# Optimization experiments

Measured on AMD Instinct MI355X. Metric: run time of the kernel, lower is better.

The kernel has to match this reference:

```python
import jax, jax.numpy as jnp
import numpy as np

B, N, C = 16, 577, 768
H, D = 12, 64
HID = 3072
EPS = 1e-5


def setup_inputs() -> dict:
    key = jax.random.key(0)
    ks = jax.random.split(key, 5)
    s = 0.02
    return {
        "x": jax.random.normal(ks[0], (B, N, C), jnp.float32),
        "w_qkv": jax.random.normal(ks[1], (C, 3 * C), jnp.float32) * s,
        "b_qkv": jnp.zeros((3 * C,), jnp.float32),
        "w_proj": jax.random.normal(ks[2], (C, C), jnp.float32) * s,
        "b_proj": jnp.zeros((C,), jnp.float32),
        "g1": jnp.ones((C,), jnp.float32),
        "be1": jnp.zeros((C,), jnp.float32),
        "g2": jnp.ones((C,), jnp.float32),
        "be2": jnp.zeros((C,), jnp.float32),
        "w1": jax.random.normal(ks[3], (C, HID), jnp.float32) * s,
        "b1": jnp.zeros((HID,), jnp.float32),
        "w2": jax.random.normal(ks[4], (HID, C), jnp.float32) * s,
        "b2": jnp.zeros((C,), jnp.float32),
    }


def _layernorm(x, g, b):
    mu = jnp.mean(x, axis=-1, keepdims=True)
    var = jnp.mean(jnp.square(x - mu), axis=-1, keepdims=True)
    return (x - mu) * jax.lax.rsqrt(var + EPS) * g + b


def reference(x, w_qkv, b_qkv, w_proj, b_proj, g1, be1, g2, be2, w1, b1, w2, b2):
    # --- pre-norm MHA ---
    xn = _layernorm(x, g1, be1)
    qkv = xn @ w_qkv + b_qkv                      # [B,N,3C]
    qkv = qkv.reshape(B, N, 3, H, D).transpose(2, 0, 3, 1, 4)  # [3,B,H,N,D]
    q, k, v = qkv[0], qkv[1], qkv[2]
    scale = 1.0 / jnp.sqrt(jnp.float32(D))
    scores = jnp.einsum("bhnd,bhmd->bhnm", q, k) * scale
    attn_weights = jax.nn.softmax(scores, axis=-1)  # [B,H,N,N]
    ctx = jnp.einsum("bhnm,bhmd->bhnd", attn_weights, v)
    ctx = ctx.transpose(0, 2, 1, 3).reshape(B, N, C)
    attn_out = ctx @ w_proj + b_proj
    x = x + attn_out
    # --- MLP (exact GELU, matching nn.GELU default) ---
    h = _layernorm(x, g2, be2) @ w1 + b1
    h = jax.nn.gelu(h, approximate=False)
    x = x + (h @ w2 + b2)
    return x, attn_weights
```

## Files before the change

### kernel.cpp

```cpp
#include <hip/hip_runtime.h>
#include <hip/hip_bf16.h>
#include <cmath>

constexpr int B_ = 16, N_ = 577, C_ = 768, H_ = 12, D_ = 64, HID_ = 3072;
constexpr int ROWS_ = B_ * N_;
constexpr int BH_ = B_ * H_;
constexpr int KVT_ = 10;
constexpr int QBLK_ = 10;

typedef __attribute__((ext_vector_type(8))) __bf16 bf16x8;
typedef __attribute__((ext_vector_type(4))) float f32x4;
typedef __attribute__((ext_vector_type(4), aligned(4))) float f32x4u;

#define DEVI __device__ __forceinline__

DEVI unsigned short f2bf(float f) {
  unsigned u = __float_as_uint(f);
  return (unsigned short)((u + 0x7fffu + ((u >> 16) & 1u)) >> 16);
}
DEVI float bf2f(unsigned short u) { return __uint_as_float(((unsigned)u) << 16); }

DEVI void gload16(const void* src, void* dst) {
  __builtin_amdgcn_global_load_lds(
      (const __attribute__((address_space(1))) char*)src,
      (__attribute__((address_space(3))) char*)dst, 16, 0, 0);
}
#define VMCNT0 asm volatile("s_waitcnt vmcnt(0)" ::: "memory")
#define FENCE asm volatile("" ::: "memory")
#define RAWBAR do { FENCE; __builtin_amdgcn_s_barrier(); FENCE; } while (0)

__global__ __launch_bounds__(256) void cvtT_kernel(const float* __restrict__ in,
                                                   unsigned short* __restrict__ out,
                                                   int K, int N) {
  __shared__ float t[64][65];
  int n0 = blockIdx.x * 64, k0 = blockIdx.y * 64;
  int tx = threadIdx.x & 63, ty = threadIdx.x >> 6;
#pragma unroll
  for (int r = 0; r < 16; r++) {
    int kr = ty * 16 + r;
    t[kr][tx] = in[(long)(k0 + kr) * N + n0 + tx];
  }
  __syncthreads();
#pragma unroll
  for (int r = 0; r < 16; r++) {
    int nr = ty * 16 + r;
    out[(long)(n0 + nr) * K + k0 + tx] = f2bf(t[tx][nr]);
  }
}

__global__ __launch_bounds__(256) void ln_kernel(const float* __restrict__ x,
                                                 const float* __restrict__ g,
                                                 const float* __restrict__ be,
                                                 unsigned short* __restrict__ out) {
  int row = blockIdx.x;
  const float* xr = x + (long)row * C_;
  float v[3];
  float s = 0.f, s2 = 0.f;
#pragma unroll
  for (int j = 0; j < 3; j++) {
    int i = threadIdx.x + j * 256;
    v[j] = xr[i];
    s += v[j];
    s2 += v[j] * v[j];
  }
#pragma unroll
  for (int o = 32; o > 0; o >>= 1) {
    s += __shfl_down(s, o);
    s2 += __shfl_down(s2, o);
  }
  __shared__ float sh[8];
  int w = threadIdx.x >> 6;
  if ((threadIdx.x & 63) == 0) { sh[w] = s; sh[4 + w] = s2; }
  __syncthreads();
  s = sh[0] + sh[1] + sh[2] + sh[3];
  s2 = sh[4] + sh[5] + sh[6] + sh[7];
  float mu = s * (1.f / C_);
  float var = s2 * (1.f / C_) - mu * mu;
  float rs = rsqrtf(var + 1e-5f);
#pragma unroll
  for (int j = 0; j < 3; j++) {
    int i = threadIdx.x + j * 256;
    out[(long)row * C_ + i] = f2bf((v[j] - mu) * rs * g[i] + be[i]);
  }
}

__global__ __launch_bounds__(256) void attn_kernel(
    const unsigned short* __restrict__ qg,
    const unsigned short* __restrict__ kg,
    const unsigned short* __restrict__ vt,
    float* __restrict__ attn,
    unsigned short* __restrict__ ctx) {
  __shared__ unsigned short KVs[2][2][64][64];
  __shared__ unsigned short Ps[4][16][72];
  const int wgid = (blockIdx.x & 7) * (BH_ * QBLK_ / 8) + (blockIdx.x >> 3);
  const int bh = wgid / QBLK_, qb = wgid % QBLK_;
  const int b = bh / H_, h = bh % H_;
  const int tid = threadIdx.x, wave = tid >> 6, lane = tid & 63;
  const int l15 = lane & 15, l4 = lane >> 4;
  const int q0w = qb * 64 + wave * 16;

  const unsigned short* Qh = qg + (long)bh * N_ * D_;
  const char* Kb = (const char*)(kg + (long)bh * N_ * D_);
  const char* Vb = (const char*)(vt + (long)bh * D_ * N_);

  int qrc = q0w + l15; if (qrc >= N_) qrc = N_ - 1;
  bf16x8 qa0 = *(const bf16x8*)(Qh + (long)qrc * D_ + l4 * 8);
  bf16x8 qa1 = *(const bf16x8*)(Qh + (long)qrc * D_ + 32 + l4 * 8);

  auto stage = [&](int buf, int which, const char* g0, int rstride) {
#pragma unroll
    for (int i = 0; i < 2; i++) {
      int off = i * 4096 + tid * 16;
      int row = off >> 7, colD = off & 127;
      const char* src = g0 + (long)row * rstride + (colD ^ ((row & 7) << 4));
      char* dst = ((char*)KVs) + buf * 16384 + which * 8192 + i * 4096 + wave * 1024;
      gload16(src, dst);
    }
  };
  auto rdKV = [&](int buf, int which, int row, int colb) -> bf16x8 {
    const char* p = ((const char*)KVs) + buf * 16384 + which * 8192 + row * 128 +
                    (colb ^ ((row & 7) << 4));
    return *(const bf16x8*)p;
  };
  auto computeS = [&](int buf, int kv0, f32x4 (&s)[4]) {
#pragma unroll
    for (int nf = 0; nf < 4; nf++) {
      int row = nf * 16 + l15;
      bf16x8 k0v = rdKV(buf, 0, row, l4 * 16);
      bf16x8 k1v = rdKV(buf, 0, row, 64 + l4 * 16);
      f32x4 z = {0.f, 0.f, 0.f, 0.f};
      z = __builtin_amdgcn_mfma_f32_16x16x32_bf16(qa0, k0v, z, 0, 0, 0);
      z = __builtin_amdgcn_mfma_f32_16x16x32_bf16(qa1, k1v, z, 0, 0, 0);
      if (kv0 + row >= N_) z = f32x4{-1e30f, -1e30f, -1e30f, -1e30f};
      s[nf] = z;
    }
  };

  float m_ln[4], l_ln[4];
#pragma unroll
  for (int r = 0; r < 4; r++) { m_ln[r] = -1e30f; l_ln[r] = 0.f; }

  stage(0, 0, Kb, 128);
  VMCNT0; __syncthreads();
  int buf = 0;
  for (int kt = 0; kt < KVT_; kt++) {
    if (kt + 1 < KVT_) stage(buf ^ 1, 0, Kb + (long)(kt + 1) * 8192, 128);
    f32x4 s[4];
    computeS(buf, kt * 64, s);
#pragma unroll
    for (int r = 0; r < 4; r++) {
      float t0 = fmaxf(fmaxf(s[0][r], s[1][r]), fmaxf(s[2][r], s[3][r]));
      float mn = fmaxf(m_ln[r], t0);
      float sc = __expf(m_ln[r] - mn);
      l_ln[r] = l_ln[r] * sc + __expf(s[0][r] - mn) + __expf(s[1][r] - mn) +
                __expf(s[2][r] - mn) + __expf(s[3][r] - mn);
      m_ln[r] = mn;
    }
    VMCNT0; __syncthreads();
    buf ^= 1;
  }

  float m_run[4], inv_l[4];
#pragma unroll
  for (int r = 0; r < 4; r++) {
    float m = m_ln[r];
#pragma unroll
    for (int o = 1; o < 16; o <<= 1) m = fmaxf(m, __shfl_xor(m, o));
    float li = l_ln[r] * __expf(m_ln[r] - m);
#pragma unroll
    for (int o = 1; o < 16; o <<= 1) li += __shfl_xor(li, o);
    m_run[r] = m;
    inv_l[r] = 1.f / li;
  }

  f32x4 cacc[4];
#pragma unroll
  for (int nf = 0; nf < 4; nf++) cacc[nf] = f32x4{0.f, 0.f, 0.f, 0.f};

  stage(0, 0, Kb, 128);
  stage(0, 1, Vb, N_ * 2);
  VMCNT0; __syncthreads();
  buf = 0;
  for (int kt = 0; kt < KVT_; kt++) {
    const int kv0 = kt * 64;
    if (kt + 1 < KVT_) {
      stage(buf ^ 1, 0, Kb + (long)(kt + 1) * 8192, 128);
      stage(buf ^ 1, 1, Vb + (long)(kt + 1) * 128, N_ * 2);
    }
    f32x4 s[4];
    computeS(buf, kv0, s);
#pragma unroll
    for (int nf = 0; nf < 4; nf++)
#pragma unroll
      for (int r = 0; r < 4; r++) {
        float p = __expf(s[nf][r] - m_run[r]) * inv_l[r];
        Ps[wave][l4 * 4 + r][nf * 16 + l15] = f2bf(p);
      }
    if (kt < KVT_ - 1) {
      int prow = lane >> 4;
      int c0 = (lane & 15) * 4;
#pragma unroll
      for (int rg = 0; rg < 4; rg++) {
        int row = rg * 4 + prow;
        int qv = q0w + row;
        if (qv < N_) {
          ushort4 pb = *(const ushort4*)&Ps[wave][row][c0];
          f32x4u f;
          f[0] = bf2f(pb.x); f[1] = bf2f(pb.y); f[2] = bf2f(pb.z); f[3] = bf2f(pb.w);
          __builtin_nontemporal_store(
              f, (f32x4u*)(attn + ((long)bh * N_ + qv) * N_ + kv0 + c0));
        }
      }
    } else {
      if ((lane & 15) == 0) {
        int prow = lane >> 4;
#pragma unroll
        for (int rg = 0; rg < 4; rg++) {
          int row = rg * 4 + prow;
          int qv = q0w + row;
          if (qv < N_)
            __builtin_nontemporal_store(bf2f(Ps[wave][row][0]),
                                        attn + ((long)bh * N_ + qv) * N_ + 576);
        }
      }
    }
#pragma unroll
    for (int ks = 0; ks < 2; ks++) {
      bf16x8 pa = *(const bf16x8*)&Ps[wave][l15][ks * 32 + l4 * 8];
#pragma unroll
      for (int nf = 0; nf < 4; nf++) {
        bf16x8 vb = rdKV(buf, 1, nf * 16 + l15, ks * 64 + l4 * 16);
        cacc[nf] = __builtin_amdgcn_mfma_f32_16x16x32_bf16(pa, vb, cacc[nf], 0, 0, 0);
      }
    }
    VMCNT0; __syncthreads();
    buf ^= 1;
  }

#pragma unroll
  for (int nf = 0; nf < 4; nf++)
#pragma unroll
    for (int r = 0; r < 4; r++) {
      int qv = q0w + l4 * 4 + r;
      if (qv >= N_) continue;
      int d = nf * 16 + l15;
      ctx[((long)b * N_ + qv) * C_ + h * D_ + d] = f2bf(cacc[nf][r]);
    }
}

template <int EPI>
__global__ __launch_bounds__(256) void gemm128(
    const unsigned short* __restrict__ A,
    const unsigned short* __restrict__ BT,
    int M, int K, int Nc,
    void* __restrict__ outp, const float* __restrict__ bias,
    const float* __restrict__ resid) {
  __shared__ unsigned short As[2][128][64];
  __shared__ unsigned short Bs[2][128][64];
  const int tid = threadIdx.x, wave = tid >> 6, lane = tid & 63;
  const int l15 = lane & 15, l4 = lane >> 4;
  const long m0 = (long)blockIdx.y * 128, n0 = (long)blockIdx.x * 128;
  const int wr = (wave >> 1) * 64, wc = (wave & 1) * 64;

  f32x4 acc[4][4];
#pragma unroll
  for (int i = 0; i < 4; i++)
#pragma unroll
    for (int j = 0; j < 4; j++) acc[i][j] = f32x4{0.f, 0.f, 0.f, 0.f};

  auto stageA = [&](int buf, int t) {
#pragma unroll
    for (int i = 0; i < 4; i++) {
      int off = i * 4096 + tid * 16;
      int row = off >> 7, colD = off & 127;
      long gr = m0 + row; if (gr >= M) gr = M - 1;
      const char* src = (const char*)A + (gr * (long)K + (long)t * 64) * 2 +
                        (colD ^ ((row & 7) << 4));
      char* dst = ((char*)As) + buf * 16384 + i * 4096 + wave * 1024;
      gload16(src, dst);
    }
  };
  auto stageB = [&](int buf, int t) {
#pragma unroll
    for (int i = 0; i < 4; i++) {
      int off = i * 4096 + tid * 16;
      int row = off >> 7, colD = off & 127;
      const char* src = (const char*)BT + ((n0 + row) * (long)K + (long)t * 64) * 2 +
                        (colD ^ ((row & 7) << 4));
      char* dst = ((char*)Bs) + buf * 16384 + i * 4096 + wave * 1024;
      gload16(src, dst);
    }
  };

  const int nt = K / 64;
  stageA(0, 0); stageB(0, 0);
  VMCNT0; __syncthreads();
  int buf = 0;
  for (int t = 0; t < nt; t++) {
    if (t + 1 < nt) { stageA(buf ^ 1, t + 1); stageB(buf ^ 1, t + 1); }
    bf16x8 af[4][2], bfr[4][2];
#pragma unroll
    for (int mf = 0; mf < 4; mf++)
#pragma unroll
      for (int kk = 0; kk < 2; kk++) {
        int row = wr + mf * 16 + l15, colb = kk * 64 + l4 * 16;
        af[mf][kk] = *(const bf16x8*)(((const char*)As) + buf * 16384 + row * 128 +
                                      (colb ^ ((row & 7) << 4)));
      }
#pragma unroll
    for (int nf = 0; nf < 4; nf++)
#pragma unroll
      for (int kk = 0; kk < 2; kk++) {
        int row = wc + nf * 16 + l15, colb = kk * 64 + l4 * 16;
        bfr[nf][kk] = *(const bf16x8*)(((const char*)Bs) + buf * 16384 + row * 128 +
                                       (colb ^ ((row & 7) << 4)));
      }
#pragma unroll
    for (int kk = 0; kk < 2; kk++)
#pragma unroll
      for (int mf = 0; mf < 4; mf++)
#pragma unroll
        for (int nf = 0; nf < 4; nf++)
          acc[mf][nf] =
              __builtin_amdgcn_mfma_f32_16x16x32_bf16(af[mf][kk], bfr[nf][kk], acc[mf][nf], 0, 0, 0);
    VMCNT0; __syncthreads();
    buf ^= 1;
  }

#pragma unroll
  for (int mf = 0; mf < 4; mf++)
#pragma unroll
    for (int nf = 0; nf < 4; nf++)
#pragma unroll
      for (int r = 0; r < 4; r++) {
        long row = m0 + wr + mf * 16 + l4 * 4 + r;
        long col = n0 + wc + nf * 16 + l15;
        if (row >= M) continue;
        float v = acc[mf][nf][r];
        if constexpr (EPI == 3 || EPI == 5) {
          float* o = (float*)outp;
          long idx = row * (long)Nc + col;
          o[idx] = v + bias[col] + resid[idx];
        } else if constexpr (EPI == 4) {
          v += bias[col];
          float ge = 0.5f * v * (1.f + erff(v * 0.70710678118654752f));
          ((unsigned short*)outp)[row * (long)Nc + col] = f2bf(ge);
        }
      }
}

template <int EPI>
__global__ __launch_bounds__(512, 2) void gemm256(
    const unsigned short* __restrict__ A,
    const unsigned short* __restrict__ BT,
    int M, int K, int Nc,
    void* __restrict__ outp, const float* __restrict__ bias,
    const float* __restrict__ resid) {
  __shared__ unsigned short smem[2][2][2][128][64];
  const int tid = threadIdx.x, wave = tid >> 6, lane = tid & 63;
  const int l15 = lane & 15, l4 = lane >> 4;
  const int wm = wave >> 2, wn = wave & 3;

  const int nbx = gridDim.x;
  const int nwg = nbx * gridDim.y;
  int orig = blockIdx.y * nbx + blockIdx.x;
  int qq = nwg >> 3, r8 = nwg & 7;
  int xcd = orig & 7, idx = orig >> 3;
  int wg = (xcd < r8 ? xcd * (qq + 1) : r8 * (qq + 1) + (xcd - r8) * qq) + idx;
  const long m0 = (long)(wg / nbx) * 256;
  const long n0 = (long)(wg % nbx) * 256;

  f32x4 acc[2][2][4][2];
#pragma unroll
  for (int a = 0; a < 2; a++)
#pragma unroll
    for (int b = 0; b < 2; b++)
#pragma unroll
      for (int m = 0; m < 4; m++)
#pragma unroll
        for (int n = 0; n < 2; n++) acc[a][b][m][n] = f32x4{0.f, 0.f, 0.f, 0.f};

  auto stage = [&](int d, int op, int half, int t) {
#pragma unroll
    for (int it = 0; it < 2; it++) {
      int off = it * 8192 + tid * 16;
      int lrow = off >> 7, colb = off & 127;
      long grow;
      if (op == 0) {
        grow = m0 + half * 128 + lrow;
        if (grow >= M) grow = M - 1;
      } else {
        grow = n0 + half * 128 + lrow;
      }
      const unsigned short* gp = (op == 0) ? A : BT;
      const char* src = (const char*)(gp + grow * (long)K + (long)t * 64) +
                        (colb ^ ((lrow & 7) << 4));
      char* dst = ((char*)smem) + (((d * 2 + op) * 2 + half) * 16384) + off;
      gload16(src, dst);
    }
  };
  auto rdfrag = [&](int d, int op, int half, int lr, int kk) -> bf16x8 {
    const char* p = ((const char*)smem) + (((d * 2 + op) * 2 + half) * 16384) + lr * 128 +
                    ((kk * 64 + l4 * 16) ^ ((lr & 7) << 4));
    return *(const bf16x8*)p;
  };

  bf16x8 av[4][2];

#define PHASE(d, qm, qn, STAGECODE, VMCODE)                                              \
  {                                                                                      \
    if constexpr (qn == 0) {                                                             \
      _Pragma("unroll") for (int m = 0; m < 4; m++)                                      \
          _Pragma("unroll") for (int kk = 0; kk < 2; kk++)                               \
              av[m][kk] = rdfrag(d, 0, qm, wm * 64 + m * 16 + l15, kk);                  \
    }                                                                                    \
    bf16x8 bv[2][2];                                                                     \
    _Pragma("unroll") for (int n = 0; n < 2; n++)                                        \
        _Pragma("unroll") for (int kk = 0; kk < 2; kk++)                                 \
            bv[n][kk] = rdfrag(d, 1, qn, wn * 32 + n * 16 + l15, kk);                    \
    STAGECODE;                                                                           \
    VMCODE;                                                                              \
    RAWBAR;                                                                              \
    __builtin_amdgcn_s_setprio(1);                                                       \
    _Pragma("unroll") for (int kk = 0; kk < 2; kk++)                                     \
        _Pragma("unroll") for (int m = 0; m < 4; m++)                                    \
            _Pragma("unroll") for (int n = 0; n < 2; n++)                                \
                acc[qm][qn][m][n] = __builtin_amdgcn_mfma_f32_16x16x32_bf16(             \
                    av[m][kk], bv[n][kk], acc[qm][qn][m][n], 0, 0, 0);                   \
    __builtin_amdgcn_s_setprio(0);                                                       \
    RAWBAR;                                                                              \
  }

  const int nt = K / 64, ni = nt / 2;
  stage(0, 0, 0, 0); stage(0, 0, 1, 0); stage(0, 1, 0, 0); stage(0, 1, 1, 0);
  stage(1, 0, 0, 1); stage(1, 0, 1, 1); stage(1, 1, 0, 1); stage(1, 1, 1, 1);
  asm volatile("s_waitcnt vmcnt(8)" ::: "memory");
  RAWBAR;

  for (int i = 0; i < ni; i++) {
    const int t1 = 2 * i + 1, t2 = 2 * i + 2, t3 = 2 * i + 3;
    PHASE(0, 0, 0, { if (i > 0) stage(1, 0, 1, t1); }, {});
    PHASE(0, 0, 1, { if (i > 0) stage(1, 1, 1, t1); }, {});
    PHASE(0, 1, 0, { if (t2 < nt) stage(0, 0, 0, t2); }, {});
    PHASE(0, 1, 1, { if (t2 < nt) stage(0, 1, 0, t2); },
          { if (t2 < nt) { asm volatile("s_waitcnt vmcnt(4)" ::: "memory"); }
            else { asm volatile("s_waitcnt vmcnt(0)" ::: "memory"); } });
    PHASE(1, 0, 0, { if (t2 < nt) stage(0, 0, 1, t2); }, {});
    PHASE(1, 0, 1, { if (t2 < nt) stage(0, 1, 1, t2); }, {});
    PHASE(1, 1, 0, { if (t3 < nt) stage(1, 0, 0, t3); }, {});
    PHASE(1, 1, 1, { if (t3 < nt) stage(1, 1, 0, t3); },
          { if (t3 < nt) { asm volatile("s_waitcnt vmcnt(4)" ::: "memory"); }
            else { asm volatile("s_waitcnt vmcnt(0)" ::: "memory"); } });
  }
#undef PHASE

#pragma unroll
  for (int qm = 0; qm < 2; qm++)
#pragma unroll
    for (int qn = 0; qn < 2; qn++)
#pragma unroll
      for (int m = 0; m < 4; m++)
#pragma unroll
        for (int n = 0; n < 2; n++)
#pragma unroll
          for (int r = 0; r < 4; r++) {
            long row = m0 + qm * 128 + wm * 64 + m * 16 + l4 * 4 + r;
            long col = n0 + qn * 128 + wn * 32 + n * 16 + l15;
            if (row >= M) continue;
            float v = acc[qm][qn][m][n][r];
            if constexpr (EPI == 0) {
              v += bias[col];
              int which = (int)col / C_;
              int rem = (int)col % C_;
              int hh = rem >> 6, d = rem & 63;
              int bb = (int)row / N_, nn = (int)row % N_;
              if (which == 0) v *= 0.125f;
              unsigned short* o = (unsigned short*)outp;
              long base = (long)which * ((long)BH_ * N_ * D_);
              long oidx;
              if (which < 2)
                oidx = base + (((long)(bb * H_ + hh)) * N_ + nn) * D_ + d;
              else
                oidx = base + (((long)(bb * H_ + hh)) * D_ + d) * N_ + nn;
              o[oidx] = f2bf(v);
            } else if constexpr (EPI == 4) {
              v += bias[col];
              float ge = 0.5f * v * (1.f + erff(v * 0.70710678118654752f));
              ((unsigned short*)outp)[row * (long)Nc + col] = f2bf(ge);
            } else {
              float* o = (float*)outp;
              long oidx = row * (long)Nc + col;
              o[oidx] = v + bias[col] + resid[oidx];
            }
          }
}

extern "C" void kernel_launch(void* const* d_in, const int* in_sizes, int n_in,
                              void* d_out, int out_size, void* d_ws, size_t ws_size,
                              hipStream_t stream) {
  const float* x = (const float*)d_in[0];
  const float* w_qkv = (const float*)d_in[1];
  const float* b_qkv = (const float*)d_in[2];
  const float* w_proj = (const float*)d_in[3];
  const float* b_proj = (const float*)d_in[4];
  const float* g1 = (const float*)d_in[5];
  const float* be1 = (const float*)d_in[6];
  const float* g2 = (const float*)d_in[7];
  const float* be2 = (const float*)d_in[8];
  const float* w1 = (const float*)d_in[9];
  const float* b1 = (const float*)d_in[10];
  const float* w2 = (const float*)d_in[11];
  const float* b2 = (const float*)d_in[12];

  char* ws = (char*)d_ws;
  const size_t SZ_TOK_BF = (size_t)ROWS_ * C_ * 2;
  unsigned short* xn = (unsigned short*)(ws);
  unsigned short* q = (unsigned short*)(ws + SZ_TOK_BF);
  unsigned short* v = (unsigned short*)(ws + 3 * SZ_TOK_BF);
  unsigned short* ctx = (unsigned short*)(ws + 4 * SZ_TOK_BF);
  unsigned short* hbuf = q;
  float* x1 = (float*)(ws + 5 * SZ_TOK_BF);
  unsigned short* wqkvT = (unsigned short*)(ws + 5 * SZ_TOK_BF + (size_t)ROWS_ * C_ * 4);
  unsigned short* wprojT = wqkvT + (size_t)C_ * 3 * C_;
  unsigned short* w1T = wprojT + (size_t)C_ * C_;
  unsigned short* w2T = w1T + (size_t)C_ * HID_;

  float* out_x = (float*)d_out;
  float* attn = out_x + (size_t)ROWS_ * C_;

  cvtT_kernel<<<dim3(3 * C_ / 64, C_ / 64), 256, 0, stream>>>(w_qkv, wqkvT, C_, 3 * C_);
  cvtT_kernel<<<dim3(C_ / 64, C_ / 64), 256, 0, stream>>>(w_proj, wprojT, C_, C_);
  cvtT_kernel<<<dim3(HID_ / 64, C_ / 64), 256, 0, stream>>>(w1, w1T, C_, HID_);
  cvtT_kernel<<<dim3(C_ / 64, HID_ / 64), 256, 0, stream>>>(w2, w2T, HID_, C_);

  ln_kernel<<<ROWS_, 256, 0, stream>>>(x, g1, be1, xn);

  {
    dim3 g(3 * C_ / 256, (ROWS_ + 255) / 256);
    gemm256<0><<<g, 512, 0, stream>>>(xn, wqkvT, ROWS_, C_, 3 * C_, q, b_qkv, nullptr);
  }
  attn_kernel<<<BH_ * QBLK_, 256, 0, stream>>>(q, q + (size_t)BH_ * N_ * D_, v, attn, ctx);
  {
    dim3 g(C_ / 128, (ROWS_ + 127) / 128);
    gemm128<3><<<g, 256, 0, stream>>>(ctx, wprojT, ROWS_, C_, C_, x1, b_proj, x);
  }
  ln_kernel<<<ROWS_, 256, 0, stream>>>(x1, g2, be2, xn);
  {
    dim3 g(HID_ / 256, (ROWS_ + 255) / 256);
    gemm256<4><<<g, 512, 0, stream>>>(xn, w1T, ROWS_, C_, HID_, hbuf, b1, nullptr);
  }
  {
    dim3 g(C_ / 128, (ROWS_ + 127) / 128);
    gemm128<5><<<g, 256, 0, stream>>>(hbuf, w2T, ROWS_, HID_, C_, out_x, b2, x1);
  }
}
```

Before: 490.1 us.

## Keep attention scores in registers to skip second QK^T pass

Stores all QK^T score tiles for a wave's 16 query rows in registers (10x4 f32x4) during the first pass. The second pass then reuses them instead of restaging K and recomputing the MFMAs, and only V is streamed. LDS use is halved and the kernel asks for 2 blocks per CU. Attention probabilities are now written directly from registers in fp32 with scattered per-lane stores instead of coalesced 16-byte stores from LDS, which changes the store pattern and may raise register pressure or cause spills.

```diff
diff --git a/kernel.cpp b/kernel.cpp
--- a/kernel.cpp
+++ b/kernel.cpp
@@ -10,7 +10,6 @@
 
 typedef __attribute__((ext_vector_type(8))) __bf16 bf16x8;
 typedef __attribute__((ext_vector_type(4))) float f32x4;
-typedef __attribute__((ext_vector_type(4), aligned(4))) float f32x4u;
 
 #define DEVI __device__ __forceinline__
 
@@ -18,7 +17,6 @@
   unsigned u = __float_as_uint(f);
   return (unsigned short)((u + 0x7fffu + ((u >> 16) & 1u)) >> 16);
 }
-DEVI float bf2f(unsigned short u) { return __uint_as_float(((unsigned)u) << 16); }
 
 DEVI void gload16(const void* src, void* dst) {
   __builtin_amdgcn_global_load_lds(
@@ -84,13 +82,13 @@
   }
 }
 
-__global__ __launch_bounds__(256) void attn_kernel(
+__global__ __launch_bounds__(256, 2) void attn_kernel(
     const unsigned short* __restrict__ qg,
     const unsigned short* __restrict__ kg,
     const unsigned short* __restrict__ vt,
     float* __restrict__ attn,
     unsigned short* __restrict__ ctx) {
-  __shared__ unsigned short KVs[2][2][64][64];
+  __shared__ unsigned short KVs[2][64][64];
   __shared__ unsigned short Ps[4][16][72];
   const int wgid = (blockIdx.x & 7) * (BH_ * QBLK_ / 8) + (blockIdx.x >> 3);
   const int bh = wgid / QBLK_, qb = wgid % QBLK_;
@@ -107,121 +105,100 @@
   bf16x8 qa0 = *(const bf16x8*)(Qh + (long)qrc * D_ + l4 * 8);
   bf16x8 qa1 = *(const bf16x8*)(Qh + (long)qrc * D_ + 32 + l4 * 8);
 
-  auto stage = [&](int buf, int which, const char* g0, int rstride) {
+  auto stage = [&](int buf, const char* g0, long rstride) {
 #pragma unroll
     for (int i = 0; i < 2; i++) {
       int off = i * 4096 + tid * 16;
       int row = off >> 7, colD = off & 127;
       const char* src = g0 + (long)row * rstride + (colD ^ ((row & 7) << 4));
-      char* dst = ((char*)KVs) + buf * 16384 + which * 8192 + i * 4096 + wave * 1024;
+      char* dst = ((char*)KVs) + buf * 8192 + i * 4096 + wave * 1024;
       gload16(src, dst);
     }
   };
-  auto rdKV = [&](int buf, int which, int row, int colb) -> bf16x8 {
-    const char* p = ((const char*)KVs) + buf * 16384 + which * 8192 + row * 128 +
+  auto rdT = [&](int buf, int row, int colb) -> bf16x8 {
+    const char* p = ((const char*)KVs) + buf * 8192 + row * 128 +
                     (colb ^ ((row & 7) << 4));
     return *(const bf16x8*)p;
   };
-  auto computeS = [&](int buf, int kv0, f32x4 (&s)[4]) {
+
+  f32x4 s_all[KVT_][4];
+  float m_ln[4];
+#pragma unroll
+  for (int r = 0; r < 4; r++) m_ln[r] = -1e30f;
+
+  stage(0, Kb, 128);
+  VMCNT0; __syncthreads();
+#pragma unroll
+  for (int kt = 0; kt < KVT_; kt++) {
+    const int buf = kt & 1;
+    if (kt + 1 < KVT_) stage(buf ^ 1, Kb + (long)(kt + 1) * 8192, 128);
 #pragma unroll
     for (int nf = 0; nf < 4; nf++) {
       int row = nf * 16 + l15;
-      bf16x8 k0v = rdKV(buf, 0, row, l4 * 16);
-      bf16x8 k1v = rdKV(buf, 0, row, 64 + l4 * 16);
+      bf16x8 k0v = rdT(buf, row, l4 * 16);
+      bf16x8 k1v = rdT(buf, row, 64 + l4 * 16);
       f32x4 z = {0.f, 0.f, 0.f, 0.f};
       z = __builtin_amdgcn_mfma_f32_16x16x32_bf16(qa0, k0v, z, 0, 0, 0);
       z = __builtin_amdgcn_mfma_f32_16x16x32_bf16(qa1, k1v, z, 0, 0, 0);
-      if (kv0 + row >= N_) z = f32x4{-1e30f, -1e30f, -1e30f, -1e30f};
-      s[nf] = z;
-    }
-  };
-
-  float m_ln[4], l_ln[4];
-#pragma unroll
-  for (int r = 0; r < 4; r++) { m_ln[r] = -1e30f; l_ln[r] = 0.f; }
-
-  stage(0, 0, Kb, 128);
-  VMCNT0; __syncthreads();
-  int buf = 0;
-  for (int kt = 0; kt < KVT_; kt++) {
-    if (kt + 1 < KVT_) stage(buf ^ 1, 0, Kb + (long)(kt + 1) * 8192, 128);
-    f32x4 s[4];
-    computeS(buf, kt * 64, s);
-#pragma unroll
-    for (int r = 0; r < 4; r++) {
-      float t0 = fmaxf(fmaxf(s[0][r], s[1][r]), fmaxf(s[2][r], s[3][r]));
-      float mn = fmaxf(m_ln[r], t0);
-      float sc = __expf(m_ln[r] - mn);
-      l_ln[r] = l_ln[r] * sc + __expf(s[0][r] - mn) + __expf(s[1][r] - mn) +
-                __expf(s[2][r] - mn) + __expf(s[3][r] - mn);
-      m_ln[r] = mn;
-    }
+      if (kt * 64 + row >= N_) z = f32x4{-1e30f, -1e30f, -1e30f, -1e30f};
+      s_all[kt][nf] = z;
+    }
+#pragma unroll
+    for (int r = 0; r < 4; r++)
+      m_ln[r] = fmaxf(m_ln[r], fmaxf(fmaxf(s_all[kt][0][r], s_all[kt][1][r]),
+                                     fmaxf(s_all[kt][2][r], s_all[kt][3][r])));
     VMCNT0; __syncthreads();
-    buf ^= 1;
-  }
-
-  float m_run[4], inv_l[4];
+  }
+
+  stage(0, Vb, N_ * 2);
+
+  float m_run[4], inv_l[4], l_ln[4];
 #pragma unroll
   for (int r = 0; r < 4; r++) {
     float m = m_ln[r];
 #pragma unroll
     for (int o = 1; o < 16; o <<= 1) m = fmaxf(m, __shfl_xor(m, o));
-    float li = l_ln[r] * __expf(m_ln[r] - m);
+    m_run[r] = m;
+    l_ln[r] = 0.f;
+  }
+#pragma unroll
+  for (int kt = 0; kt < KVT_; kt++)
+#pragma unroll
+    for (int nf = 0; nf < 4; nf++)
+#pragma unroll
+      for (int r = 0; r < 4; r++) {
+        float e = __expf(s_all[kt][nf][r] - m_run[r]);
+        s_all[kt][nf][r] = e;
+        l_ln[r] += e;
+      }
+#pragma unroll
+  for (int r = 0; r < 4; r++) {
+    float li = l_ln[r];
 #pragma unroll
     for (int o = 1; o < 16; o <<= 1) li += __shfl_xor(li, o);
-    m_run[r] = m;
     inv_l[r] = 1.f / li;
   }
+  VMCNT0; __syncthreads();
 
   f32x4 cacc[4];
 #pragma unroll
   for (int nf = 0; nf < 4; nf++) cacc[nf] = f32x4{0.f, 0.f, 0.f, 0.f};
 
-  stage(0, 0, Kb, 128);
-  stage(0, 1, Vb, N_ * 2);
-  VMCNT0; __syncthreads();
-  buf = 0;
+#pragma unroll
   for (int kt = 0; kt < KVT_; kt++) {
+    const int buf = kt & 1;
     const int kv0 = kt * 64;
-    if (kt + 1 < KVT_) {
-      stage(buf ^ 1, 0, Kb + (long)(kt + 1) * 8192, 128);
-      stage(buf ^ 1, 1, Vb + (long)(kt + 1) * 128, N_ * 2);
-    }
-    f32x4 s[4];
-    computeS(buf, kv0, s);
-#pragma unroll
-    for (int nf = 0; nf < 4; nf++)
+    if (kt + 1 < KVT_) stage(buf ^ 1, Vb + (long)(kt + 1) * 128, N_ * 2);
+#pragma unroll
+    for (int nf = 0; nf < 4; nf++) {
+      int kvcol = kv0 + nf * 16 + l15;
 #pragma unroll
       for (int r = 0; r < 4; r++) {
-        float p = __expf(s[nf][r] - m_run[r]) * inv_l[r];
+        float p = s_all[kt][nf][r] * inv_l[r];
+        int qv = q0w + l4 * 4 + r;
+        if (qv < N_ && kvcol < N_)
+          __builtin_nontemporal_store(p, attn + ((long)bh * N_ + qv) * N_ + kvcol);
         Ps[wave][l4 * 4 + r][nf * 16 + l15] = f2bf(p);
-      }
-    if (kt < KVT_ - 1) {
-      int prow = lane >> 4;
-      int c0 = (lane & 15) * 4;
-#pragma unroll
-      for (int rg = 0; rg < 4; rg++) {
-        int row = rg * 4 + prow;
-        int qv = q0w + row;
-        if (qv < N_) {
-          ushort4 pb = *(const ushort4*)&Ps[wave][row][c0];
-          f32x4u f;
-          f[0] = bf2f(pb.x); f[1] = bf2f(pb.y); f[2] = bf2f(pb.z); f[3] = bf2f(pb.w);
-          __builtin_nontemporal_store(
-              f, (f32x4u*)(attn + ((long)bh * N_ + qv) * N_ + kv0 + c0));
-        }
-      }
-    } else {
-      if ((lane & 15) == 0) {
-        int prow = lane >> 4;
-#pragma unroll
-        for (int rg = 0; rg < 4; rg++) {
-          int row = rg * 4 + prow;
-          int qv = q0w + row;
-          if (qv < N_)
-            __builtin_nontemporal_store(bf2f(Ps[wave][row][0]),
-                                        attn + ((long)bh * N_ + qv) * N_ + 576);
-        }
       }
     }
 #pragma unroll
@@ -229,12 +206,11 @@
       bf16x8 pa = *(const bf16x8*)&Ps[wave][l15][ks * 32 + l4 * 8];
 #pragma unroll
       for (int nf = 0; nf < 4; nf++) {
-        bf16x8 vb = rdKV(buf, 1, nf * 16 + l15, ks * 64 + l4 * 16);
+        bf16x8 vb = rdT(buf, nf * 16 + l15, ks * 64 + l4 * 16);
         cacc[nf] = __builtin_amdgcn_mfma_f32_16x16x32_bf16(pa, vb, cacc[nf], 0, 0, 0);
       }
     }
     VMCNT0; __syncthreads();
-    buf ^= 1;
   }
 
 #pragma unroll
```

New measurement: 585.1 us. +19.4%, slower.

## Triple-buffer attention K/V tiles with prefetch distance two and partial vmcnt waits

Applied to the files above, without the earlier changes.

The attention kernel's LDS staging for K and V moves from double to triple buffering, and tiles are now prefetched two iterations ahead. The full vmcnt(0)-plus-barrier at the end of each iteration is replaced by a counted s_waitcnt before a single barrier at the top of the loop. The wait counts take the in-flight attention-weight stores into account. The aim is to overlap more global-to-LDS load latency with the QK and PV MFMA work. In exchange it uses more LDS, which could lower occupancy, and it relies on hand-tuned wait counts that are fragile if the store count changes.

```diff
diff --git a/kernel.cpp b/kernel.cpp
--- a/kernel.cpp
+++ b/kernel.cpp
@@ -26,6 +26,7 @@
       (__attribute__((address_space(3))) char*)dst, 16, 0, 0);
 }
 #define VMCNT0 asm volatile("s_waitcnt vmcnt(0)" ::: "memory")
+#define VMW(n) asm volatile("s_waitcnt vmcnt(" #n ")" ::: "memory")
 #define FENCE asm volatile("" ::: "memory")
 #define RAWBAR do { FENCE; __builtin_amdgcn_s_barrier(); FENCE; } while (0)
 
@@ -90,7 +91,8 @@
     const unsigned short* __restrict__ vt,
     float* __restrict__ attn,
     unsigned short* __restrict__ ctx) {
-  __shared__ unsigned short KVs[2][2][64][64];
+  __shared__ unsigned short Ks[3][64][64];
+  __shared__ unsigned short Vs[3][64][64];
   __shared__ unsigned short Ps[4][16][72];
   const int wgid = (blockIdx.x & 7) * (BH_ * QBLK_ / 8) + (blockIdx.x >> 3);
   const int bh = wgid / QBLK_, qb = wgid % QBLK_;
@@ -107,27 +109,37 @@
   bf16x8 qa0 = *(const bf16x8*)(Qh + (long)qrc * D_ + l4 * 8);
   bf16x8 qa1 = *(const bf16x8*)(Qh + (long)qrc * D_ + 32 + l4 * 8);
 
-  auto stage = [&](int buf, int which, const char* g0, int rstride) {
-#pragma unroll
-    for (int i = 0; i < 2; i++) {
-      int off = i * 4096 + tid * 16;
-      int row = off >> 7, colD = off & 127;
-      const char* src = g0 + (long)row * rstride + (colD ^ ((row & 7) << 4));
-      char* dst = ((char*)KVs) + buf * 16384 + which * 8192 + i * 4096 + wave * 1024;
-      gload16(src, dst);
-    }
-  };
-  auto rdKV = [&](int buf, int which, int row, int colb) -> bf16x8 {
-    const char* p = ((const char*)KVs) + buf * 16384 + which * 8192 + row * 128 +
-                    (colb ^ ((row & 7) << 4));
-    return *(const bf16x8*)p;
-  };
-  auto computeS = [&](int buf, int kv0, f32x4 (&s)[4]) {
+  auto srcAddr = [&](const char* g0, long rstride, int i) -> const char* {
+    int off = i * 4096 + tid * 16;
+    int row = off >> 7, colD = off & 127;
+    return g0 + (long)row * rstride + (colD ^ ((row & 7) << 4));
+  };
+  auto stageK = [&](int bu, int kt) {
+    const char* g0 = Kb + (long)kt * 8192;
+#pragma unroll
+    for (int i = 0; i < 2; i++)
+      gload16(srcAddr(g0, 128, i), ((char*)Ks) + bu * 8192 + i * 4096 + wave * 1024);
+  };
+  auto stageV = [&](int bu, int kt) {
+    const char* g0 = Vb + (long)kt * 128;
+#pragma unroll
+    for (int i = 0; i < 2; i++)
+      gload16(srcAddr(g0, (long)N_ * 2, i), ((char*)Vs) + bu * 8192 + i * 4096 + wave * 1024);
+  };
+  auto rdK = [&](int bu, int row, int colb) -> bf16x8 {
+    return *(const bf16x8*)(((const char*)Ks) + bu * 8192 + row * 128 +
+                            (colb ^ ((row & 7) << 4)));
+  };
+  auto rdV = [&](int bu, int row, int colb) -> bf16x8 {
+    return *(const bf16x8*)(((const char*)Vs) + bu * 8192 + row * 128 +
+                            (colb ^ ((row & 7) << 4)));
+  };
+  auto computeS = [&](int bu, int kv0, f32x4 (&s)[4]) {
 #pragma unroll
     for (int nf = 0; nf < 4; nf++) {
       int row = nf * 16 + l15;
-      bf16x8 k0v = rdKV(buf, 0, row, l4 * 16);
-      bf16x8 k1v = rdKV(buf, 0, row, 64 + l4 * 16);
+      bf16x8 k0v = rdK(bu, row, l4 * 16);
+      bf16x8 k1v = rdK(bu, row, 64 + l4 * 16);
       f32x4 z = {0.f, 0.f, 0.f, 0.f};
       z = __builtin_amdgcn_mfma_f32_16x16x32_bf16(qa0, k0v, z, 0, 0, 0);
       z = __builtin_amdgcn_mfma_f32_16x16x32_bf16(qa1, k1v, z, 0, 0, 0);
@@ -140,13 +152,15 @@
 #pragma unroll
   for (int r = 0; r < 4; r++) { m_ln[r] = -1e30f; l_ln[r] = 0.f; }
 
-  stage(0, 0, Kb, 128);
-  VMCNT0; __syncthreads();
-  int buf = 0;
+  stageK(0, 0); stageK(1, 1);
+#pragma unroll
   for (int kt = 0; kt < KVT_; kt++) {
-    if (kt + 1 < KVT_) stage(buf ^ 1, 0, Kb + (long)(kt + 1) * 8192, 128);
+    const int bu = kt % 3;
+    if (kt < KVT_ - 1) { VMW(2); } else { VMW(0); }
+    RAWBAR;
+    if (kt + 2 < KVT_) stageK((kt + 2) % 3, kt + 2);
     f32x4 s[4];
-    computeS(buf, kt * 64, s);
+    computeS(bu, kt * 64, s);
 #pragma unroll
     for (int r = 0; r < 4; r++) {
       float t0 = fmaxf(fmaxf(s[0][r], s[1][r]), fmaxf(s[2][r], s[3][r]));
@@ -156,9 +170,10 @@
                 __expf(s[2][r] - mn) + __expf(s[3][r] - mn);
       m_ln[r] = mn;
     }
-    VMCNT0; __syncthreads();
-    buf ^= 1;
-  }
+  }
+
+  RAWBAR;
+  stageK(0, 0); stageV(0, 0); stageK(1, 1); stageV(1, 1);
 
   float m_run[4], inv_l[4];
 #pragma unroll
@@ -177,18 +192,18 @@
 #pragma unroll
   for (int nf = 0; nf < 4; nf++) cacc[nf] = f32x4{0.f, 0.f, 0.f, 0.f};
 
-  stage(0, 0, Kb, 128);
-  stage(0, 1, Vb, N_ * 2);
-  VMCNT0; __syncthreads();
-  buf = 0;
+#pragma unroll
   for (int kt = 0; kt < KVT_; kt++) {
+    const int bu = kt % 3;
     const int kv0 = kt * 64;
-    if (kt + 1 < KVT_) {
-      stage(buf ^ 1, 0, Kb + (long)(kt + 1) * 8192, 128);
-      stage(buf ^ 1, 1, Vb + (long)(kt + 1) * 128, N_ * 2);
-    }
+    if (kt == 0) { VMW(4); }
+    else if (kt == 1) { VMW(8); }
+    else if (kt < KVT_ - 1) { VMW(12); }
+    else { VMW(8); }
+    RAWBAR;
+    if (kt + 2 < KVT_) { stageK((kt + 2) % 3, kt + 2); stageV((kt + 2) % 3, kt + 2); }
     f32x4 s[4];
-    computeS(buf, kv0, s);
+    computeS(bu, kv0, s);
 #pragma unroll
     for (int nf = 0; nf < 4; nf++)
 #pragma unroll
@@ -229,12 +244,10 @@
       bf16x8 pa = *(const bf16x8*)&Ps[wave][l15][ks * 32 + l4 * 8];
 #pragma unroll
       for (int nf = 0; nf < 4; nf++) {
-        bf16x8 vb = rdKV(buf, 1, nf * 16 + l15, ks * 64 + l4 * 16);
+        bf16x8 vb = rdV(bu, nf * 16 + l15, ks * 64 + l4 * 16);
         cacc[nf] = __builtin_amdgcn_mfma_f32_16x16x32_bf16(pa, vb, cacc[nf], 0, 0, 0);
       }
     }
-    VMCNT0; __syncthreads();
-    buf ^= 1;
   }
 
 #pragma unroll
```

After: 484.2 us. No clear change (-1.2%).
